# Kernel tuning notes

Measured on AMD Instinct MI355X. Metric: run time of the kernel, lower is better.

The kernel has to match this reference:

```python
import jax, jax.numpy as jnp
import numpy as np


def setup_inputs() -> dict:
    key = jax.random.key(0)
    image = jax.random.randint(key, (4, 2048, 2048), 0, 50000, dtype=jnp.int32)
    return {"image": image}


def reference(image) -> jnp.ndarray:
    # Faithful, single-pass equivalent of LabelGapAdjustment(shift=False).
    # The original while-loop (decrement labels above each missing label until
    # labels are the consecutive set 1..K) is exactly dense-rank remapping:
    # new_label = 1-based rank of the label among the sorted unique labels.
    imin = image.min()
    image_shift = 1 - imin
    shifted = jnp.where(imin <= 0, image + image_shift, image)

    flat = shifted.reshape(-1)
    order = jnp.argsort(flat)
    s = flat[order]  # sorted labels
    # 1 where a new distinct value starts; cumsum -> 1-based dense rank
    is_new = jnp.concatenate(
        [jnp.ones((1,), dtype=jnp.int32), (s[1:] != s[:-1]).astype(jnp.int32)]
    )
    ranks_sorted = jnp.cumsum(is_new)  # [N], values 1..K
    # scatter ranks back to original positions
    ranks = jnp.zeros_like(flat).at[order].set(ranks_sorted.astype(flat.dtype))
    compact = ranks.reshape(image.shape)

    # shift=False: undo the shift (original subtracts image_shift unconditionally)
    return compact - image_shift
```

## Files before the change

### kernel.cpp

```cpp
#include <hip/hip_runtime.h>
#include <limits.h>

#define TABLE 65536
#define NBITW (TABLE / 32)
#define NTAB  512
#define CHUNK 16
#define MIN_OFF 0
#define BITS_OFF 64
#define PACK_OFF (64 + NBITW)
#define TAB_OFF  (PACK_OFF + 2 * NBITW)

__global__ __launch_bounds__(1024) void lga_mark_kernel(const int* __restrict__ img,
                                                        int n, int n4, int* ws) {
    __shared__ unsigned char tbl[TABLE];
    unsigned int* tbl32 = (unsigned int*)tbl;
    int t = threadIdx.x;
    for (int i = t; i < TABLE / 4; i += 1024) tbl32[i] = 0;
    if (blockIdx.x == 0) {
        for (int i = t; i < NBITW; i += 1024) ws[BITS_OFF + i] = 0;
    }
    __syncthreads();

    int stride = gridDim.x * blockDim.x;
    for (int i = blockIdx.x * blockDim.x + t; i < n4; i += stride) {
        int4 v = ((const int4*)img)[i];
        tbl[v.x] = 1;
        tbl[v.y] = 1;
        tbl[v.z] = 1;
        tbl[v.w] = 1;
    }
    if (blockIdx.x == 0 && t == 0) {
        for (int j = n4 * 4; j < n; ++j) tbl[img[j]] = 1;
    }
    __syncthreads();

    unsigned int* mytab = (unsigned int*)(ws + TAB_OFF) + blockIdx.x * NBITW;
    for (int d = t; d < NBITW; d += 1024) {
        const unsigned int* p = tbl32 + d * 8;
        unsigned int m = 0;
        #pragma unroll
        for (int j = 0; j < 8; ++j) {
            unsigned int w = p[j];
            m |= (w & 1u) << (j * 4);
            m |= ((w >> 8) & 1u) << (j * 4 + 1);
            m |= ((w >> 16) & 1u) << (j * 4 + 2);
            m |= ((w >> 24) & 1u) << (j * 4 + 3);
        }
        mytab[d] = m;
    }
}

__global__ __launch_bounds__(128) void lga_merge_kernel(int* ws) {
    int d = blockIdx.x * 128 + threadIdx.x;
    const unsigned int* tabs = (const unsigned int*)(ws + TAB_OFF)
                             + (size_t)blockIdx.y * CHUNK * NBITW;
    unsigned int m = 0;
    #pragma unroll
    for (int k = 0; k < CHUNK; ++k) m |= tabs[k * NBITW + d];
    if (m) atomicOr((unsigned int*)(ws + BITS_OFF) + d, m);
}

__global__ __launch_bounds__(1024) void lga_scan_kernel(int* ws) {
    const unsigned int* bits = (const unsigned int*)(ws + BITS_OFF);
    uint4* pack = (uint4*)(ws + PACK_OFF);
    int t = threadIdx.x;
    int lane = t & 63;
    int wave = t >> 6;

    unsigned int d0 = bits[2 * t], d1 = bits[2 * t + 1];
    int c0 = __popc(d0);
    int s = c0 + __popc(d1);
    int firstset;
    if (d0)      firstset = 64 * t + __ffs(d0) - 1;
    else if (d1) firstset = 64 * t + 32 + __ffs(d1) - 1;
    else         firstset = INT_MAX;

    int v = s;
    #pragma unroll
    for (int off = 1; off < 64; off <<= 1) {
        int u = __shfl_up(v, off, 64);
        if (lane >= off) v += u;
    }
    int fm = firstset;
    #pragma unroll
    for (int off = 32; off > 0; off >>= 1)
        fm = min(fm, __shfl_down(fm, off, 64));

    __shared__ int wsum[16];
    __shared__ int wmin[16];
    if (lane == 63) wsum[wave] = v;
    if (lane == 0)  wmin[wave] = fm;
    __syncthreads();
    if (wave == 0 && lane < 16) {
        int w = wsum[lane];
        #pragma unroll
        for (int off = 1; off < 16; off <<= 1) {
            int u = __shfl_up(w, off, 16);
            if (lane >= off) w += u;
        }
        wsum[lane] = w;
        int m = wmin[lane];
        #pragma unroll
        for (int off = 8; off > 0; off >>= 1)
            m = min(m, __shfl_down(m, off, 16));
        if (lane == 0) ws[MIN_OFF] = m;
    }
    __syncthreads();

    unsigned int excl = (unsigned int)(v - s + (wave > 0 ? wsum[wave - 1] : 0));
    pack[t] = make_uint4(excl, d0, excl + (unsigned int)c0, d1);
}

__global__ __launch_bounds__(1024) void lga_remap_kernel(const int* __restrict__ img,
                                                         int* __restrict__ out,
                                                         int n, int n4,
                                                         const int* __restrict__ ws) {
    __shared__ uint2 lp[NBITW];
    const uint2* pack = (const uint2*)(ws + PACK_OFF);
    int t = threadIdx.x;
    for (int i = t; i < NBITW; i += 1024) lp[i] = pack[i];
    int imin = ws[MIN_OFF];
    __syncthreads();

    int stride = gridDim.x * blockDim.x;
    for (int i = blockIdx.x * blockDim.x + t; i < n4; i += stride) {
        int4 v = ((const int4*)img)[i];
        int4 r;
        {
            uint2 p = lp[((unsigned)v.x) >> 5];
            r.x = (int)(p.x + __popc(p.y & ((1u << (v.x & 31)) - 1u))) + imin;
        }
        {
            uint2 p = lp[((unsigned)v.y) >> 5];
            r.y = (int)(p.x + __popc(p.y & ((1u << (v.y & 31)) - 1u))) + imin;
        }
        {
            uint2 p = lp[((unsigned)v.z) >> 5];
            r.z = (int)(p.x + __popc(p.y & ((1u << (v.z & 31)) - 1u))) + imin;
        }
        {
            uint2 p = lp[((unsigned)v.w) >> 5];
            r.w = (int)(p.x + __popc(p.y & ((1u << (v.w & 31)) - 1u))) + imin;
        }
        ((int4*)out)[i] = r;
    }
    if (blockIdx.x == 0 && t == 0) {
        for (int j = n4 * 4; j < n; ++j) {
            unsigned v = (unsigned)img[j];
            uint2 p = lp[v >> 5];
            out[j] = (int)(p.x + __popc(p.y & ((1u << (v & 31)) - 1u))) + imin;
        }
    }
}

extern "C" void kernel_launch(void* const* d_in, const int* in_sizes, int n_in,
                              void* d_out, int out_size, void* d_ws, size_t ws_size,
                              hipStream_t stream) {
    const int* img = (const int*)d_in[0];
    int* out = (int*)d_out;
    int* ws = (int*)d_ws;
    int n = in_sizes[0];
    int n4 = n / 4;

    lga_mark_kernel<<<NTAB, 1024, 0, stream>>>(img, n, n4, ws);
    lga_merge_kernel<<<dim3(NBITW / 128, NTAB / CHUNK), 128, 0, stream>>>(ws);
    lga_scan_kernel<<<1, 1024, 0, stream>>>(ws);
    lga_remap_kernel<<<512, 1024, 0, stream>>>(img, out, n, n4, ws);
}
```

Before: 126.9 us.

## Replace atomic merge with partial tables, vectorize writes, nontemporal remap stores

The merge step no longer clears a global bitmap and uses atomicOr. Each chunk now writes its own partial table, and the scan kernel ORs the 32 partials together. Table writes and merge reads are vectorized to 128 bits. The remap loop is unrolled by two and uses nontemporal stores so the large output does not pollute the cache. In exchange, the single-block scan kernel now reads 32 times more data.

```diff
diff --git a/kernel.cpp b/kernel.cpp
--- a/kernel.cpp
+++ b/kernel.cpp
@@ -5,10 +5,13 @@
 #define NBITW (TABLE / 32)
 #define NTAB  512
 #define CHUNK 16
+#define NCHUNK (NTAB / CHUNK)
 #define MIN_OFF 0
-#define BITS_OFF 64
-#define PACK_OFF (64 + NBITW)
-#define TAB_OFF  (PACK_OFF + 2 * NBITW)
+#define PACK_OFF 64
+#define PART_OFF (PACK_OFF + 2 * NBITW)
+#define TAB_OFF  (PART_OFF + NCHUNK * NBITW)
+
+typedef int ivec4 __attribute__((ext_vector_type(4)));
 
 __global__ __launch_bounds__(1024) void lga_mark_kernel(const int* __restrict__ img,
                                                         int n, int n4, int* ws) {
@@ -16,14 +19,11 @@
     unsigned int* tbl32 = (unsigned int*)tbl;
     int t = threadIdx.x;
     for (int i = t; i < TABLE / 4; i += 1024) tbl32[i] = 0;
-    if (blockIdx.x == 0) {
-        for (int i = t; i < NBITW; i += 1024) ws[BITS_OFF + i] = 0;
-    }
     __syncthreads();
 
     int stride = gridDim.x * blockDim.x;
     for (int i = blockIdx.x * blockDim.x + t; i < n4; i += stride) {
-        int4 v = ((const int4*)img)[i];
+        ivec4 v = ((const ivec4*)img)[i];
         tbl[v.x] = 1;
         tbl[v.y] = 1;
         tbl[v.z] = 1;
@@ -34,40 +34,54 @@
     }
     __syncthreads();
 
-    unsigned int* mytab = (unsigned int*)(ws + TAB_OFF) + blockIdx.x * NBITW;
-    for (int d = t; d < NBITW; d += 1024) {
-        const unsigned int* p = tbl32 + d * 8;
-        unsigned int m = 0;
+    if (t < NBITW / 4) {
+        uint4* mytab = (uint4*)((unsigned int*)(ws + TAB_OFF) + blockIdx.x * NBITW);
+        unsigned int m[4];
         #pragma unroll
-        for (int j = 0; j < 8; ++j) {
-            unsigned int w = p[j];
-            m |= (w & 1u) << (j * 4);
-            m |= ((w >> 8) & 1u) << (j * 4 + 1);
-            m |= ((w >> 16) & 1u) << (j * 4 + 2);
-            m |= ((w >> 24) & 1u) << (j * 4 + 3);
+        for (int q = 0; q < 4; ++q) {
+            const unsigned int* p = tbl32 + (4 * t + q) * 8;
+            unsigned int mm = 0;
+            #pragma unroll
+            for (int j = 0; j < 8; ++j) {
+                unsigned int w = p[j];
+                mm |= (w & 1u) << (j * 4);
+                mm |= ((w >> 8) & 1u) << (j * 4 + 1);
+                mm |= ((w >> 16) & 1u) << (j * 4 + 2);
+                mm |= ((w >> 24) & 1u) << (j * 4 + 3);
+            }
+            m[q] = mm;
         }
-        mytab[d] = m;
+        mytab[t] = make_uint4(m[0], m[1], m[2], m[3]);
     }
 }
 
 __global__ __launch_bounds__(128) void lga_merge_kernel(int* ws) {
-    int d = blockIdx.x * 128 + threadIdx.x;
-    const unsigned int* tabs = (const unsigned int*)(ws + TAB_OFF)
-                             + (size_t)blockIdx.y * CHUNK * NBITW;
-    unsigned int m = 0;
+    int d4 = blockIdx.x * 128 + threadIdx.x;
+    const uint4* tabs = (const uint4*)((const unsigned int*)(ws + TAB_OFF)
+                                       + (size_t)blockIdx.y * CHUNK * NBITW);
+    unsigned int m0 = 0, m1 = 0, m2 = 0, m3 = 0;
     #pragma unroll
-    for (int k = 0; k < CHUNK; ++k) m |= tabs[k * NBITW + d];
-    if (m) atomicOr((unsigned int*)(ws + BITS_OFF) + d, m);
+    for (int k = 0; k < CHUNK; ++k) {
+        uint4 v = tabs[k * (NBITW / 4) + d4];
+        m0 |= v.x; m1 |= v.y; m2 |= v.z; m3 |= v.w;
+    }
+    uint4* part = (uint4*)((unsigned int*)(ws + PART_OFF) + (size_t)blockIdx.y * NBITW);
+    part[d4] = make_uint4(m0, m1, m2, m3);
 }
 
 __global__ __launch_bounds__(1024) void lga_scan_kernel(int* ws) {
-    const unsigned int* bits = (const unsigned int*)(ws + BITS_OFF);
+    const unsigned int* part = (const unsigned int*)(ws + PART_OFF);
     uint4* pack = (uint4*)(ws + PACK_OFF);
     int t = threadIdx.x;
     int lane = t & 63;
     int wave = t >> 6;
 
-    unsigned int d0 = bits[2 * t], d1 = bits[2 * t + 1];
+    unsigned int d0 = 0, d1 = 0;
+    #pragma unroll
+    for (int c = 0; c < NCHUNK; ++c) {
+        d0 |= part[c * NBITW + 2 * t];
+        d1 |= part[c * NBITW + 2 * t + 1];
+    }
     int c0 = __popc(d0);
     int s = c0 + __popc(d1);
     int firstset;
@@ -122,35 +136,35 @@
     int imin = ws[MIN_OFF];
     __syncthreads();
 
+    int tid = blockIdx.x * blockDim.x + t;
     int stride = gridDim.x * blockDim.x;
-    for (int i = blockIdx.x * blockDim.x + t; i < n4; i += stride) {
-        int4 v = ((const int4*)img)[i];
-        int4 r;
-        {
-            uint2 p = lp[((unsigned)v.x) >> 5];
-            r.x = (int)(p.x + __popc(p.y & ((1u << (v.x & 31)) - 1u))) + imin;
-        }
-        {
-            uint2 p = lp[((unsigned)v.y) >> 5];
-            r.y = (int)(p.x + __popc(p.y & ((1u << (v.y & 31)) - 1u))) + imin;
-        }
-        {
-            uint2 p = lp[((unsigned)v.z) >> 5];
-            r.z = (int)(p.x + __popc(p.y & ((1u << (v.z & 31)) - 1u))) + imin;
-        }
-        {
-            uint2 p = lp[((unsigned)v.w) >> 5];
-            r.w = (int)(p.x + __popc(p.y & ((1u << (v.w & 31)) - 1u))) + imin;
-        }
-        ((int4*)out)[i] = r;
+
+    #define RANK1(vv) ({ uint2 _p = lp[((unsigned)(vv)) >> 5]; \
+                         (int)(_p.x + __popc(_p.y & ((1u << ((vv) & 31)) - 1u))) + imin; })
+
+    int i = tid;
+    for (; i + stride < n4; i += 2 * stride) {
+        ivec4 va = ((const ivec4*)img)[i];
+        ivec4 vb = ((const ivec4*)img)[i + stride];
+        ivec4 ra, rb;
+        ra.x = RANK1(va.x); ra.y = RANK1(va.y); ra.z = RANK1(va.z); ra.w = RANK1(va.w);
+        rb.x = RANK1(vb.x); rb.y = RANK1(vb.y); rb.z = RANK1(vb.z); rb.w = RANK1(vb.w);
+        __builtin_nontemporal_store(ra, (ivec4*)out + i);
+        __builtin_nontemporal_store(rb, (ivec4*)out + i + stride);
+    }
+    if (i < n4) {
+        ivec4 va = ((const ivec4*)img)[i];
+        ivec4 ra;
+        ra.x = RANK1(va.x); ra.y = RANK1(va.y); ra.z = RANK1(va.z); ra.w = RANK1(va.w);
+        __builtin_nontemporal_store(ra, (ivec4*)out + i);
     }
     if (blockIdx.x == 0 && t == 0) {
         for (int j = n4 * 4; j < n; ++j) {
-            unsigned v = (unsigned)img[j];
-            uint2 p = lp[v >> 5];
-            out[j] = (int)(p.x + __popc(p.y & ((1u << (v & 31)) - 1u))) + imin;
+            int vv = img[j];
+            out[j] = RANK1(vv);
         }
     }
+    #undef RANK1
 }
 
 extern "C" void kernel_launch(void* const* d_in, const int* in_sizes, int n_in,
@@ -163,7 +177,7 @@
     int n4 = n / 4;
 
     lga_mark_kernel<<<NTAB, 1024, 0, stream>>>(img, n, n4, ws);
-    lga_merge_kernel<<<dim3(NBITW / 128, NTAB / CHUNK), 128, 0, stream>>>(ws);
+    lga_merge_kernel<<<dim3(NBITW / 512, NCHUNK), 128, 0, stream>>>(ws);
     lga_scan_kernel<<<1, 1024, 0, stream>>>(ws);
     lga_remap_kernel<<<512, 1024, 0, stream>>>(img, out, n, n4, ws);
 }
```

Measured after the change: 128.8 us. No clear change (+1.5%).
